# Optimization experiments

Hardware: AMD Instinct MI355X
Metric: run time of the kernel (lower is better)

Reference implementation:

```python
import jax, jax.numpy as jnp
import numpy as np
import math

# Config: 8 packed images, each a 32x32 patch grid (t=1) -> equal seglen 1024
NSEG, GH, GW = 8, 32, 32
L = GH * GW            # 1024 tokens per segment
S = NSEG * L           # 8192 packed tokens
H, NH = 1024, 16
HD = H // NH           # 64, head dim (rope dim), divisible by 4
MLP = 4096
THETA = 10000.0


def _make_rope_cos_sin():
    # Rope2DPosEmb._precompute_freqs_cis for a (GH, GW) grid, dim=HD
    flat = np.arange(L, dtype=np.float32)
    x_pos = flat % GW
    y_pos = flat // GW
    dim_range = np.arange(0, HD, 4, dtype=np.float32)[: HD // 4]
    freqs = 1.0 / THETA ** (dim_range / HD)          # [HD//4]
    x_f = np.outer(x_pos, freqs)                     # [L, HD//4]
    y_f = np.outer(y_pos, freqs)
    # interleave x/y angles per frequency -> [L, HD//2]
    ang = np.stack([x_f, y_f], axis=-1).reshape(L, HD // 2)
    ang = np.tile(ang, (NSEG, 1))                    # same grid repeated per image
    return jnp.asarray(np.cos(ang)), jnp.asarray(np.sin(ang))


def setup_inputs() -> dict:
    key = jax.random.key(0)
    ks = jax.random.split(key, 8)
    cos, sin = _make_rope_cos_sin()
    inp = {
        "x": jax.random.normal(ks[0], (S, H), jnp.float32),
        "wqkv": jax.random.normal(ks[1], (3 * H, H), jnp.float32) * math.sqrt(1.0 / H),
        "wo": jax.random.normal(ks[2], (H, H), jnp.float32) * math.sqrt(1.0 / H),
        "ln0_g": jnp.ones((H,), jnp.float32),
        "ln0_b": jnp.zeros((H,), jnp.float32),
        "ln1_g": jnp.ones((H,), jnp.float32),
        "ln1_b": jnp.zeros((H,), jnp.float32),
        "fc0_w": jax.random.normal(ks[3], (MLP, H), jnp.float32) * math.sqrt(2.0 / H),
        "fc0_b": jnp.zeros((MLP,), jnp.float32),
        "fc1_w": jax.random.normal(ks[4], (H, MLP), jnp.float32) * math.sqrt(2.0 / MLP),
        "fc1_b": jnp.zeros((H,), jnp.float32),
        "rope_cos": cos,
        "rope_sin": sin,
        "cu_seqlens": jnp.arange(NSEG + 1, dtype=jnp.int32) * L,
    }
    return inp


def _layernorm(x, g, b, eps=1e-5):
    m = x.mean(-1, keepdims=True)
    v = ((x - m) ** 2).mean(-1, keepdims=True)
    return (x - m) * jax.lax.rsqrt(v + eps) * g + b


def _apply_rope(x, cos, sin):
    # x: [S, NH, HD]; cos/sin: [S, HD//2]. Complex mult on (even, odd) pairs.
    xr = x.reshape(S, NH, HD // 2, 2)
    x0, x1 = xr[..., 0], xr[..., 1]
    c = cos[:, None, :]
    s = sin[:, None, :]
    o0 = x0 * c - x1 * s
    o1 = x0 * s + x1 * c
    return jnp.stack([o0, o1], axis=-1).reshape(S, NH, HD)


def reference(x, wqkv, wo, ln0_g, ln0_b, ln1_g, ln1_b,
              fc0_w, fc0_b, fc1_w, fc1_b, rope_cos, rope_sin, cu_seqlens):
    # --- attention branch (pre-norm) ---
    h = _layernorm(x, ln0_g, ln0_b)
    qkv = (h @ wqkv.T).reshape(S, 3, NH, HD)
    q, k, v = qkv[:, 0], qkv[:, 1], qkv[:, 2]
    q = _apply_rope(q, rope_cos, rope_sin)
    k = _apply_rope(k, rope_cos, rope_sin)
    # block-diagonal varlen attention: equal-length segments -> reshape
    qb = q.reshape(NSEG, L, NH, HD)
    kb = k.reshape(NSEG, L, NH, HD)
    vb = v.reshape(NSEG, L, NH, HD)
    scores = jnp.einsum("blhd,bmhd->bhlm", qb, kb) / math.sqrt(HD)
    p = jax.nn.softmax(scores.astype(jnp.float32), axis=-1).astype(x.dtype)
    attn = jnp.einsum("bhlm,bmhd->blhd", p, vb).reshape(S, H)
    x = x + attn @ wo.T
    # --- MLP branch (pre-norm) ---
    h2 = _layernorm(x, ln1_g, ln1_b)
    mlp = jax.nn.gelu(h2 @ fc0_w.T + fc0_b, approximate=False) @ fc1_w.T + fc1_b
    return x + mlp
```

## Files before the change

kernel.cpp:

```cpp
#include <hip/hip_runtime.h>
#include <math.h>


typedef __bf16 bf16x8 __attribute__((ext_vector_type(8)));
typedef float f32x4 __attribute__((ext_vector_type(4)));
typedef float f32x16 __attribute__((ext_vector_type(16)));
typedef unsigned int u32;

__device__ __forceinline__ unsigned short f2b(float f) {
  unsigned u = __float_as_uint(f);
  return (unsigned short)((u + 0x7FFFu + ((u >> 16) & 1u)) >> 16);
}
__device__ __forceinline__ float b2f(unsigned short h) {
  return __uint_as_float(((unsigned)h) << 16);
}
__device__ __forceinline__ void async_ld16(const void* g, void* l) {
  __builtin_amdgcn_global_load_lds((__attribute__((address_space(1))) void*)g,
                                   (__attribute__((address_space(3))) void*)l,
                                   16, 0, 0);
}
__device__ __forceinline__ float exp2fast(float x) {
#if __has_builtin(__builtin_amdgcn_exp2f)
  return __builtin_amdgcn_exp2f(x);
#else
  return exp2f(x);
#endif
}
__device__ __forceinline__ float rcpfast(float x) {
#if __has_builtin(__builtin_amdgcn_rcpf)
  return __builtin_amdgcn_rcpf(x);
#else
  return 1.0f / x;
#endif
}

__global__ __launch_bounds__(256) void castln_kernel(
    const float* __restrict__ w0, const float* __restrict__ w1,
    const float* __restrict__ w2, const float* __restrict__ w3,
    unsigned short* __restrict__ wdst,
    const float* __restrict__ x, const float* __restrict__ g,
    const float* __restrict__ bt, unsigned short* __restrict__ hout) {
  __shared__ float red[8];
  const int blk = blockIdx.x;
  if (blk < 12288) {
    const int t = blk * 256 + threadIdx.x;
    const float* src;
    int off;
    if (t < 786432) { src = w0; off = t; }
    else if (t < 1048576) { src = w1; off = t - 786432; }
    else if (t < 2097152) { src = w2; off = t - 1048576; }
    else { src = w3; off = t - 2097152; }
    const float4 v = ((const float4*)src)[off];
    ushort4 o;
    o.x = f2b(v.x); o.y = f2b(v.y); o.z = f2b(v.z); o.w = f2b(v.w);
    ((ushort4*)wdst)[t] = o;
    return;
  }
  const int row = blk - 12288, t = threadIdx.x;
  const float4 v = ((const float4*)(x + (size_t)row * 1024))[t];
  float s = v.x + v.y + v.z + v.w;
  float s2 = v.x * v.x + v.y * v.y + v.z * v.z + v.w * v.w;
#pragma unroll
  for (int m = 1; m < 64; m <<= 1) {
    s += __shfl_xor(s, m, 64);
    s2 += __shfl_xor(s2, m, 64);
  }
  if ((t & 63) == 0) { red[t >> 6] = s; red[4 + (t >> 6)] = s2; }
  __syncthreads();
  const float ts = red[0] + red[1] + red[2] + red[3];
  const float ts2 = red[4] + red[5] + red[6] + red[7];
  const float mean = ts * (1.f / 1024.f);
  const float var = ts2 * (1.f / 1024.f) - mean * mean;
  const float inv = rsqrtf(var + 1e-5f);
  const float4 gv = ((const float4*)g)[t];
  const float4 bv = ((const float4*)bt)[t];
  ushort4 o;
  o.x = f2b((v.x - mean) * inv * gv.x + bv.x);
  o.y = f2b((v.y - mean) * inv * gv.y + bv.y);
  o.z = f2b((v.z - mean) * inv * gv.z + bv.z);
  o.w = f2b((v.w - mean) * inv * gv.w + bv.w);
  ((ushort4*)hout)[(size_t)row * 256 + t] = o;
}

__global__ __launch_bounds__(256) void ln_kernel(const float* __restrict__ x,
                                                 const float* __restrict__ g,
                                                 const float* __restrict__ bt,
                                                 unsigned short* __restrict__ out) {
  __shared__ float red[8];
  const int row = blockIdx.x, t = threadIdx.x;
  const float4 v = ((const float4*)(x + (size_t)row * 1024))[t];
  float s = v.x + v.y + v.z + v.w;
  float s2 = v.x * v.x + v.y * v.y + v.z * v.z + v.w * v.w;
#pragma unroll
  for (int m = 1; m < 64; m <<= 1) {
    s += __shfl_xor(s, m, 64);
    s2 += __shfl_xor(s2, m, 64);
  }
  if ((t & 63) == 0) { red[t >> 6] = s; red[4 + (t >> 6)] = s2; }
  __syncthreads();
  const float ts = red[0] + red[1] + red[2] + red[3];
  const float ts2 = red[4] + red[5] + red[6] + red[7];
  const float mean = ts * (1.f / 1024.f);
  const float var = ts2 * (1.f / 1024.f) - mean * mean;
  const float inv = rsqrtf(var + 1e-5f);
  const float4 gv = ((const float4*)g)[t];
  const float4 bv = ((const float4*)bt)[t];
  ushort4 o;
  o.x = f2b((v.x - mean) * inv * gv.x + bv.x);
  o.y = f2b((v.y - mean) * inv * gv.y + bv.y);
  o.z = f2b((v.z - mean) * inv * gv.z + bv.z);
  o.w = f2b((v.w - mean) * inv * gv.w + bv.w);
  ((ushort4*)out)[(size_t)row * 256 + t] = o;
}

template <int MODE, int NBN, int BM>
__global__ __launch_bounds__(512, 2) void gemm_p8(
    const unsigned short* __restrict__ A, const unsigned short* __restrict__ B,
    int M, int N, int K, float* __restrict__ outf, unsigned short* __restrict__ outb,
    const float* __restrict__ res, const float* __restrict__ bias) {
  constexpr int NPH = (BM == 256) ? 4 : 2;
  constexpr int NF = (BM == 256) ? 2 : 4;
  constexpr int M_REP = BM / 32;
  constexpr int AI = BM / 128;
  constexpr int STG2 = (BM == 256) ? 2 : 1;
  __shared__ __align__(16) unsigned short As[2][2][BM * 32];
  __shared__ __align__(16) unsigned short Bs[2][2][256 * 32];
  const int bid = blockIdx.x;
  const int j8 = bid & 7, g = bid >> 3;
  const int bm = ((g / NBN) * 8 + j8) * BM;
  const int bn = (g % NBN) * 256;
  const int t = threadIdx.x, wave = t >> 6, lane = t & 63;
  const int quad = lane >> 4, l16 = lane & 15;
  const int wm = (wave >> 2) * (M_REP * 16);
  const int wn = (wave & 3) * 64;
  const int r16 = lane >> 2;
  const int cs8 = (((lane & 3) ^ ((lane >> 3) & 3)) * 8);
  const unsigned short* AgS[AI];
  unsigned short* AlS[AI];
#pragma unroll
  for (int i = 0; i < AI; i++) {
    const int r0 = wave * (AI * 16) + i * 16;
    AgS[i] = A + (size_t)(bm + r0 + r16) * K + cs8;
    AlS[i] = &As[0][0][r0 * 32];
  }
  const unsigned short* BgS[2];
  unsigned short* BlS[2];
#pragma unroll
  for (int i = 0; i < 2; i++) {
    const int r0 = wave * 32 + i * 16;
    BgS[i] = B + (size_t)(bn + r0 + r16) * K + cs8;
    BlS[i] = &Bs[0][0][r0 * 32];
  }
#define STG(bi, kt, ks)                                                      \
  do {                                                                       \
    _Pragma("unroll") for (int i_ = 0; i_ < AI; i_++)                        \
        async_ld16(AgS[i_] + (size_t)(kt) * 64 + (ks) * 32,                  \
                   AlS[i_] + ((bi) * 2 + (ks)) * (BM * 32));                 \
    _Pragma("unroll") for (int i_ = 0; i_ < 2; i_++)                         \
        async_ld16(BgS[i_] + (size_t)(kt) * 64 + (ks) * 32,                  \
                   BlS[i_] + ((bi) * 2 + (ks)) * (256 * 32));                \
  } while (0)

  f32x4 acc[M_REP][4] = {};
  const int NT = K >> 6;
  const int rq = ((quad ^ ((l16 >> 1) & 3)) * 8);
  STG(0, 0, 0);
  STG(0, 0, 1);
  STG(1, 1, 0);
  __builtin_amdgcn_sched_barrier(0);
  if (BM == 256) asm volatile("s_waitcnt vmcnt(4)" ::: "memory");
  else           asm volatile("s_waitcnt vmcnt(3)" ::: "memory");
  __builtin_amdgcn_sched_barrier(0);
  __builtin_amdgcn_s_barrier();
  __builtin_amdgcn_sched_barrier(0);

  bf16x8 af[M_REP];
  for (int u = 0; u < NT; ++u) {
    const int buf = u & 1, nbuf = buf ^ 1;
#pragma unroll
    for (int p = 0; p < NPH; ++p) {
      const int ks = (NPH == 4) ? (p >> 1) : p;
      const int j0 = (NPH == 4) ? (p & 1) * 2 : 0;
      const unsigned short* Ab = &As[buf][ks][0];
      const unsigned short* Bb = &Bs[buf][ks][0];
      if (NPH == 2 || (p & 1) == 0) {
#pragma unroll
        for (int i = 0; i < M_REP; i++)
          af[i] = *(const bf16x8*)(Ab + (wm + i * 16 + l16) * 32 + rq);
      }
      bf16x8 bfv[NF];
#pragma unroll
      for (int jj = 0; jj < NF; jj++)
        bfv[jj] = *(const bf16x8*)(Bb + (wn + (j0 + jj) * 16 + l16) * 32 + rq);
      if (p == 0 && u + 1 < NT) STG(nbuf, u + 1, 1);
      if (p == STG2 && u + 2 < NT) STG(buf, u + 2, 0);
      __builtin_amdgcn_sched_barrier(0);
      __builtin_amdgcn_s_barrier();
      asm volatile("s_waitcnt lgkmcnt(0)" ::: "memory");
      __builtin_amdgcn_sched_barrier(0);
      __builtin_amdgcn_s_setprio(1);
#pragma unroll
      for (int jj = 0; jj < NF; jj++)
#pragma unroll
        for (int i = 0; i < M_REP; i++)
          acc[i][j0 + jj] = __builtin_amdgcn_mfma_f32_16x16x32_bf16(
              af[i], bfv[jj], acc[i][j0 + jj], 0, 0, 0);
      __builtin_amdgcn_s_setprio(0);
      if (p == NPH - 1 && u + 1 < NT) {
        __builtin_amdgcn_sched_barrier(0);
        if (u + 2 < NT) {
          if (BM == 256) asm volatile("s_waitcnt vmcnt(4)" ::: "memory");
          else           asm volatile("s_waitcnt vmcnt(3)" ::: "memory");
        } else {
          asm volatile("s_waitcnt vmcnt(0)" ::: "memory");
        }
      }
      __builtin_amdgcn_sched_barrier(0);
      __builtin_amdgcn_s_barrier();
      __builtin_amdgcn_sched_barrier(0);
    }
  }
#undef STG
#pragma unroll
  for (int i = 0; i < M_REP; i++)
#pragma unroll
    for (int jj = 0; jj < 4; jj++)
#pragma unroll
      for (int r = 0; r < 4; r++) {
        const int m = bm + wm + i * 16 + quad * 4 + r;
        const int n = bn + wn + jj * 16 + l16;
        const size_t idx = (size_t)m * N + n;
        const float v = acc[i][jj][r];
        if (MODE == 1) {
          outf[idx] = v + res[idx];
        } else if (MODE == 2) {
          const float z = v + bias[n];
          const float u = z * (0.7978845608f + 0.03567740814f * z * z);
          const float e = fminf(u * 2.885390082f, 80.f);
          const float tt = exp2fast(e);
          outb[idx] = f2b(z * tt * rcpfast(tt + 1.0f));
        } else if (MODE == 3) {
          outf[idx] = v + bias[n] + res[idx];
        } else {
          outb[idx] = f2b(v);
        }
      }
}

template <int MODE, int NBN, int BN>
__global__ __launch_bounds__(512, 2) void gemm_bt8(
    const unsigned short* __restrict__ A, const unsigned short* __restrict__ B,
    int M, int N, int K, float* __restrict__ outf, unsigned short* __restrict__ outb,
    const float* __restrict__ res, const float* __restrict__ bias) {
  constexpr int NBI = BN / 64;
  constexpr int WN_WAVES = BN / 64;
  constexpr int WM_WAVES = 8 / WN_WAVES;
  constexpr int M_REP = (256 / WM_WAVES) / 16;
  constexpr int N_REP = 4;
  __shared__ __align__(16) unsigned short As[2][256 * 64];
  __shared__ __align__(16) unsigned short Bs[2][BN * 64];
  const int bid = blockIdx.x;
  const int j8 = bid & 7, g = bid >> 3;
  const int bm = ((g / NBN) * 8 + j8) * 256;
  const int bn = (g % NBN) * BN;
  const int t = threadIdx.x, wave = t >> 6, lane = t & 63;
  const int quad = lane >> 4, l16 = lane & 15;
  const int wm = (wave / WN_WAVES) * (M_REP * 16);
  const int wn = (wave % WN_WAVES) * 64;
  const int l8 = lane >> 3;
  const int cs = ((lane & 7) ^ (l8 & 7)) * 8;
  const unsigned short* Ag[4];
  unsigned short* Al[4];
#pragma unroll
  for (int i = 0; i < 4; i++) {
    const int r = wave * 32 + i * 8;
    Ag[i] = A + (size_t)(bm + r + l8) * K + cs;
    Al[i] = &As[0][r * 64];
  }
  const unsigned short* Bg[NBI];
  unsigned short* Bl[NBI];
#pragma unroll
  for (int i = 0; i < NBI; i++) {
    const int r = wave * (NBI * 8) + i * 8;
    Bg[i] = B + (size_t)(bn + r + l8) * K + cs;
    Bl[i] = &Bs[0][r * 64];
  }
#define STAGE(bi, k0)                                                        \
  do {                                                                       \
    _Pragma("unroll") for (int i_ = 0; i_ < 4; i_++)                         \
        async_ld16(Ag[i_] + (k0), Al[i_] + (bi) * (256 * 64));               \
    _Pragma("unroll") for (int i_ = 0; i_ < NBI; i_++)                       \
        async_ld16(Bg[i_] + (k0), Bl[i_] + (bi) * (BN * 64));                \
  } while (0)

  f32x4 acc[M_REP][N_REP] = {};
  const int NT = K >> 6;
  const int swk = l16 & 7;
  STAGE(0, 0);
  STAGE(1, 64);
  if (BN == 256) asm volatile("s_waitcnt vmcnt(8)" ::: "memory");
  else           asm volatile("s_waitcnt vmcnt(6)" ::: "memory");
  __builtin_amdgcn_sched_barrier(0);
  __builtin_amdgcn_s_barrier();
  __builtin_amdgcn_sched_barrier(0);
  int k0 = 128;
  for (int tI = 0; tI < NT; ++tI) {
    const int cur = tI & 1;
    const unsigned short* Ab = &As[cur][0];
    const unsigned short* Bb = &Bs[cur][0];
#pragma unroll
    for (int ks = 0; ks < 2; ks++) {
      bf16x8 af[M_REP], bfv[N_REP];
#pragma unroll
      for (int i = 0; i < M_REP; i++)
        af[i] = *(const bf16x8*)(Ab + (wm + i * 16 + l16) * 64 +
                                 (((ks * 4 + quad) ^ swk) * 8));
#pragma unroll
      for (int j = 0; j < N_REP; j++)
        bfv[j] = *(const bf16x8*)(Bb + (wn + j * 16 + l16) * 64 +
                                  (((ks * 4 + quad) ^ swk) * 8));
      __builtin_amdgcn_s_setprio(1);
#pragma unroll
      for (int j = 0; j < N_REP; j++)
#pragma unroll
        for (int i = 0; i < M_REP; i++)
          acc[i][j] = __builtin_amdgcn_mfma_f32_16x16x32_bf16(af[i], bfv[j],
                                                              acc[i][j], 0, 0, 0);
      __builtin_amdgcn_s_setprio(0);
    }
    if (tI + 1 == NT) break;
    __builtin_amdgcn_sched_barrier(0);
    __builtin_amdgcn_s_barrier();
    __builtin_amdgcn_sched_barrier(0);
    if (tI + 2 < NT) {
      STAGE(cur, k0);
      k0 += 64;
      if (BN == 256) asm volatile("s_waitcnt vmcnt(8)" ::: "memory");
      else           asm volatile("s_waitcnt vmcnt(6)" ::: "memory");
    } else {
      asm volatile("s_waitcnt vmcnt(0)" ::: "memory");
    }
    __builtin_amdgcn_sched_barrier(0);
    __builtin_amdgcn_s_barrier();
    __builtin_amdgcn_sched_barrier(0);
  }
#undef STAGE
#pragma unroll
  for (int i = 0; i < M_REP; i++)
#pragma unroll
    for (int j = 0; j < N_REP; j++)
#pragma unroll
      for (int r = 0; r < 4; r++) {
        const int m = bm + wm + i * 16 + quad * 4 + r;
        const int n = bn + wn + j * 16 + l16;
        const size_t idx = (size_t)m * N + n;
        const float v = acc[i][j][r];
        if (MODE == 1) {
          outf[idx] = v + res[idx];
        } else if (MODE == 2) {
          const float z = v + bias[n];
          const float u = z * (0.7978845608f + 0.03567740814f * z * z);
          const float e = fminf(u * 2.885390082f, 80.f);
          const float tt = exp2fast(e);
          outb[idx] = f2b(z * tt * rcpfast(tt + 1.0f));
        } else if (MODE == 3) {
          outf[idx] = v + bias[n] + res[idx];
        } else {
          outb[idx] = f2b(v);
        }
      }
}

__device__ __forceinline__ u32 rope2(u32 in, float c, float sn, float sc) {
  const float a = b2f((unsigned short)(in & 0xffff));
  const float b = b2f((unsigned short)(in >> 16));
  return (u32)f2b((a * c - b * sn) * sc) | ((u32)f2b((a * sn + b * c) * sc) << 16);
}
__global__ __launch_bounds__(256) void ropevt_kernel(const unsigned short* __restrict__ qkv,
                                                     const float* __restrict__ cb,
                                                     const float* __restrict__ sb,
                                                     unsigned short* __restrict__ qh,
                                                     unsigned short* __restrict__ kh,
                                                     unsigned short* __restrict__ vt) {
  __shared__ unsigned short tile[64][72];
  const int blk = blockIdx.x;
  if (blk < 4096) {
    const int tid = blk * 256 + threadIdx.x;
    const int ii = tid & 7, head = (tid >> 3) & 15, s = tid >> 7;
    const float4 cv = *(const float4*)(cb + s * 32 + ii * 4);
    const float4 sv = *(const float4*)(sb + s * 32 + ii * 4);
    const unsigned short* base = qkv + (size_t)s * 3072 + head * 64 + ii * 8;
    const uint4 qa = *(const uint4*)base;
    const uint4 ka = *(const uint4*)(base + 1024);
    const int seg = s >> 10, l = s & 1023;
    const size_t o = ((size_t)((seg * 16 + head) * 1024 + l)) * 64 + ii * 8;
    const float QSC = 0.125f * 1.44269504f;
    uint4 qo, ko;
    qo.x = rope2(qa.x, cv.x, sv.x, QSC); ko.x = rope2(ka.x, cv.x, sv.x, 1.f);
    qo.y = rope2(qa.y, cv.y, sv.y, QSC); ko.y = rope2(ka.y, cv.y, sv.y, 1.f);
    qo.z = rope2(qa.z, cv.z, sv.z, QSC); ko.z = rope2(ka.z, cv.z, sv.z, 1.f);
    qo.w = rope2(qa.w, cv.w, sv.w, QSC); ko.w = rope2(ka.w, cv.w, sv.w, 1.f);
    *(uint4*)(qh + o) = qo;
    *(uint4*)(kh + o) = ko;
    return;
  }
  const int b = blk - 4096;
  const int lt = b & 15, head = (b >> 4) & 15, seg = b >> 8;
  const int t = threadIdx.x;
  const int r = t >> 2, c0 = (t & 3) * 16;
  const unsigned short* src =
      qkv + ((size_t)(seg * 1024 + lt * 64 + r)) * 3072 + 2048 + head * 64 + c0;
#pragma unroll
  for (int k = 0; k < 16; k++) tile[r][c0 + k] = src[k];
  __syncthreads();
  unsigned short* dst =
      vt + ((size_t)((seg * 16 + head) * 64 + r)) * 1024 + lt * 64 + c0;
#pragma unroll
  for (int k = 0; k < 16; k++) dst[k] = tile[c0 + k][r];
}

__global__ __launch_bounds__(256) void attn_kernel(const unsigned short* __restrict__ qh,
                                                   const unsigned short* __restrict__ kh,
                                                   const unsigned short* __restrict__ vt,
                                                   unsigned short* __restrict__ out) {
  __shared__ __align__(16) unsigned short Qs[128 * 64];
  __shared__ __align__(16) unsigned short Ks[64 * 64];
  __shared__ __align__(16) unsigned short Vs[64 * 64];
  __shared__ float wl[128];
  const int b = blockIdx.x;
  const int head = b & 15, seg = (b >> 4) & 7, qt = b >> 7;
  const int t = threadIdx.x, wave = t >> 6, lane = t & 63;
  const int h = lane >> 5, q31 = lane & 31;
  const size_t sh = (size_t)(seg * 16 + head);
  const unsigned short* qbase = qh + (sh * 1024 + (size_t)qt * 128) * 64;
  const unsigned short* kbase = kh + sh * 1024 * 64;
  const unsigned short* vbase = vt + sh * 64 * 1024;
  const int r8 = lane >> 3;
  const int c8 = ((lane & 7) ^ (r8 & 7)) * 8;
#pragma unroll
  for (int cc = 0; cc < 4; cc++) {
    const int chunk = wave * 4 + cc;
    async_ld16(qbase + (size_t)(chunk * 8 + r8) * 64 + c8, Qs + chunk * 512);
  }
  const int qrow_l = wave * 32 + q31;
  const int qsw = qrow_l & 7;
  bf16x8 qf[4];
  float lsum = 0.f;
  f32x16 oacc[2] = {};

  for (int kt = 0; kt < 16; kt++) {
    const int ch0 = wave * 2;
    async_ld16(kbase + (size_t)(kt * 64 + ch0 * 8 + r8) * 64 + c8, Ks + ch0 * 512);
    async_ld16(kbase + (size_t)(kt * 64 + ch0 * 8 + 8 + r8) * 64 + c8, Ks + ch0 * 512 + 512);
    async_ld16(vbase + (size_t)(ch0 * 8 + r8) * 1024 + kt * 64 + c8, Vs + ch0 * 512);
    async_ld16(vbase + (size_t)(ch0 * 8 + 8 + r8) * 1024 + kt * 64 + c8, Vs + ch0 * 512 + 512);
    __syncthreads();
    if (kt == 0) {
#pragma unroll
      for (int ks = 0; ks < 4; ks++)
        qf[ks] = *(const bf16x8*)(Qs + qrow_l * 64 + (((2 * ks + h) ^ qsw)) * 8);
    }
    f32x16 st[2] = {{}, {}};
#pragma unroll
    for (int T = 0; T < 2; T++) {
      const int krow = 32 * T + q31;
      const int ksw = krow & 7;
#pragma unroll
      for (int ks = 0; ks < 4; ks++) {
        const bf16x8 kf = *(const bf16x8*)(Ks + krow * 64 + (((2 * ks + h) ^ ksw)) * 8);
        st[T] = __builtin_amdgcn_mfma_f32_32x32x16_bf16(kf, qf[ks], st[T], 0, 0, 0);
      }
    }
    u32 pk[2][4][2];
#pragma unroll
    for (int T = 0; T < 2; T++)
#pragma unroll
      for (int g = 0; g < 4; g++)
#pragma unroll
        for (int e = 0; e < 2; e++) {
          const float plo = exp2fast(st[T][4 * g + 2 * e]);
          const float phi = exp2fast(st[T][4 * g + 2 * e + 1]);
          lsum += plo + phi;
          pk[T][g][e] = (u32)f2b(plo) | ((u32)f2b(phi) << 16);
        }
    u32 rcv[2][4];
#pragma unroll
    for (int T = 0; T < 2; T++) {
      const u32 p0 = h ? pk[T][0][0] : pk[T][1][0];
      const u32 p1 = h ? pk[T][0][1] : pk[T][1][1];
      const u32 p2 = h ? pk[T][2][0] : pk[T][3][0];
      const u32 p3 = h ? pk[T][2][1] : pk[T][3][1];
      rcv[T][0] = (u32)__shfl_xor((int)p0, 32, 64);
      rcv[T][1] = (u32)__shfl_xor((int)p1, 32, 64);
      rcv[T][2] = (u32)__shfl_xor((int)p2, 32, 64);
      rcv[T][3] = (u32)__shfl_xor((int)p3, 32, 64);
    }
#pragma unroll
    for (int tt = 0; tt < 4; tt++) {
      const int T = tt >> 1, uu = tt & 1;
      union { u32 u[4]; bf16x8 v; } af;
      if (h == 0) {
        af.u[0] = pk[T][2 * uu][0];
        af.u[1] = pk[T][2 * uu][1];
        af.u[2] = rcv[T][2 * uu];
        af.u[3] = rcv[T][2 * uu + 1];
      } else {
        af.u[0] = rcv[T][2 * uu];
        af.u[1] = rcv[T][2 * uu + 1];
        af.u[2] = pk[T][2 * uu + 1][0];
        af.u[3] = pk[T][2 * uu + 1][1];
      }
#pragma unroll
      for (int ot = 0; ot < 2; ot++) {
        const int vrow = 32 * ot + q31;
        const int vsw = vrow & 7;
        const bf16x8 bv = *(const bf16x8*)(Vs + vrow * 64 + (((2 * tt + h) ^ vsw)) * 8);
        oacc[ot] = __builtin_amdgcn_mfma_f32_32x32x16_bf16(af.v, bv, oacc[ot], 0, 0, 0);
      }
    }
    __syncthreads();
  }
  lsum += __shfl_xor(lsum, 32, 64);
  if (h == 0) wl[wave * 32 + q31] = lsum;
  const int qglob = seg * 1024 + qt * 128 + wave * 32;
#pragma unroll
  for (int g = 0; g < 4; g++) {
    const float4 lv = *(const float4*)&wl[wave * 32 + 8 * g + 4 * h];
#pragma unroll
    for (int m = 0; m < 4; m++) {
      const int r16 = 4 * g + m;
      const int qrow = qglob + m + 8 * g + 4 * h;
      const float invl = rcpfast((&lv.x)[m]);
#pragma unroll
      for (int ot = 0; ot < 2; ot++)
        out[(size_t)qrow * 1024 + head * 64 + 32 * ot + q31] = f2b(oacc[ot][r16] * invl);
    }
  }
}

extern "C" void kernel_launch(void* const* d_in, const int* in_sizes, int n_in,
                              void* d_out, int out_size, void* d_ws, size_t ws_size,
                              hipStream_t stream) {
  (void)in_sizes; (void)n_in; (void)out_size; (void)ws_size;
  const float* x    = (const float*)d_in[0];
  const float* wqkv = (const float*)d_in[1];
  const float* wo   = (const float*)d_in[2];
  const float* ln0g = (const float*)d_in[3];
  const float* ln0b = (const float*)d_in[4];
  const float* ln1g = (const float*)d_in[5];
  const float* ln1b = (const float*)d_in[6];
  const float* fc0w = (const float*)d_in[7];
  const float* fc0b = (const float*)d_in[8];
  const float* fc1w = (const float*)d_in[9];
  const float* fc1b = (const float*)d_in[10];
  const float* rc   = (const float*)d_in[11];
  const float* rsn  = (const float*)d_in[12];
  float* out = (float*)d_out;
  char* w = (char*)d_ws;
  const size_t MB = 1u << 20;
  unsigned short* hb    = (unsigned short*)(w + 0);
  unsigned short* bqkv  = (unsigned short*)(w + 16 * MB);
  unsigned short* bwo   = (unsigned short*)(w + 22 * MB);
  unsigned short* bfc0  = (unsigned short*)(w + 24 * MB);
  unsigned short* bfc1  = (unsigned short*)(w + 32 * MB);
  unsigned short* qhb   = (unsigned short*)(w + 40 * MB);
  unsigned short* khb   = (unsigned short*)(w + 56 * MB);
  unsigned short* vtb   = (unsigned short*)(w + 72 * MB);
  unsigned short* attnb = (unsigned short*)(w + 88 * MB);
  unsigned short* qkvb  = (unsigned short*)(w + 104 * MB);
  unsigned short* midb  = (unsigned short*)(w + 104 * MB);

  castln_kernel<<<20480, 256, 0, stream>>>(wqkv, wo, fc0w, fc1w, bqkv,
                                           x, ln0g, ln0b, hb);
  gemm_p8<4, 12, 256><<<384, 512, 0, stream>>>(hb, bqkv, 8192, 3072, 1024,
                                               nullptr, qkvb, nullptr, nullptr);
  ropevt_kernel<<<6144, 256, 0, stream>>>(qkvb, rc, rsn, qhb, khb, vtb);
  attn_kernel<<<1024, 256, 0, stream>>>(qhb, khb, vtb, attnb);
  gemm_p8<1, 4, 128><<<256, 512, 0, stream>>>(attnb, bwo, 8192, 1024, 1024,
                                              out, nullptr, x, nullptr);
  ln_kernel<<<8192, 256, 0, stream>>>(out, ln1g, ln1b, hb);
  gemm_bt8<2, 16, 256><<<512, 512, 0, stream>>>(hb, bfc0, 8192, 4096, 1024,
                                                nullptr, midb, nullptr, fc0b);
  gemm_p8<3, 4, 128><<<256, 512, 0, stream>>>(midb, bfc1, 8192, 1024, 4096,
                                              out, nullptr, out, fc1b);
}
```

Before: 490.7 us.

## Double-buffer K/V tiles in attention kernel and load Q directly to registers

The attention kernel now keeps two LDS buffers for K and V and issues the asynchronous loads for the next key tile before computing on the current one. This overlaps global-to-LDS traffic with the MFMA and softmax work, and it replaces the two per-iteration __syncthreads with a single waitcnt plus barrier. Q fragments are read straight from global memory into registers, which removes the Q LDS staging buffer. LDS use stays about the same, and the raw barrier/waitcnt sequence has to be ordered correctly to avoid races.

```diff
diff --git a/kernel.cpp b/kernel.cpp
--- a/kernel.cpp
+++ b/kernel.cpp
@@ -423,9 +423,8 @@
                                                    const unsigned short* __restrict__ kh,
                                                    const unsigned short* __restrict__ vt,
                                                    unsigned short* __restrict__ out) {
-  __shared__ __align__(16) unsigned short Qs[128 * 64];
-  __shared__ __align__(16) unsigned short Ks[64 * 64];
-  __shared__ __align__(16) unsigned short Vs[64 * 64];
+  __shared__ __align__(16) unsigned short Ks[2 * 4096];
+  __shared__ __align__(16) unsigned short Vs[2 * 4096];
   __shared__ float wl[128];
   const int b = blockIdx.x;
   const int head = b & 15, seg = (b >> 4) & 7, qt = b >> 7;
@@ -437,29 +436,37 @@
   const unsigned short* vbase = vt + sh * 64 * 1024;
   const int r8 = lane >> 3;
   const int c8 = ((lane & 7) ^ (r8 & 7)) * 8;
-#pragma unroll
-  for (int cc = 0; cc < 4; cc++) {
-    const int chunk = wave * 4 + cc;
-    async_ld16(qbase + (size_t)(chunk * 8 + r8) * 64 + c8, Qs + chunk * 512);
-  }
+  const int ch0 = wave * 2;
+#define STAGEKV(kt, bi)                                                        \
+  do {                                                                         \
+    async_ld16(kbase + (size_t)((kt) * 64 + ch0 * 8 + r8) * 64 + c8,           \
+               Ks + (bi) * 4096 + ch0 * 512);                                  \
+    async_ld16(kbase + (size_t)((kt) * 64 + ch0 * 8 + 8 + r8) * 64 + c8,       \
+               Ks + (bi) * 4096 + ch0 * 512 + 512);                            \
+    async_ld16(vbase + (size_t)(ch0 * 8 + r8) * 1024 + (kt) * 64 + c8,         \
+               Vs + (bi) * 4096 + ch0 * 512);                                  \
+    async_ld16(vbase + (size_t)(ch0 * 8 + 8 + r8) * 1024 + (kt) * 64 + c8,     \
+               Vs + (bi) * 4096 + ch0 * 512 + 512);                            \
+  } while (0)
+
   const int qrow_l = wave * 32 + q31;
-  const int qsw = qrow_l & 7;
   bf16x8 qf[4];
+#pragma unroll
+  for (int ks = 0; ks < 4; ks++)
+    qf[ks] = *(const bf16x8*)(qbase + (size_t)qrow_l * 64 + ks * 16 + h * 8);
+  STAGEKV(0, 0);
+  asm volatile("s_waitcnt vmcnt(0)" ::: "memory");
+  __builtin_amdgcn_sched_barrier(0);
+  __builtin_amdgcn_s_barrier();
+  __builtin_amdgcn_sched_barrier(0);
+
   float lsum = 0.f;
   f32x16 oacc[2] = {};
-
   for (int kt = 0; kt < 16; kt++) {
-    const int ch0 = wave * 2;
-    async_ld16(kbase + (size_t)(kt * 64 + ch0 * 8 + r8) * 64 + c8, Ks + ch0 * 512);
-    async_ld16(kbase + (size_t)(kt * 64 + ch0 * 8 + 8 + r8) * 64 + c8, Ks + ch0 * 512 + 512);
-    async_ld16(vbase + (size_t)(ch0 * 8 + r8) * 1024 + kt * 64 + c8, Vs + ch0 * 512);
-    async_ld16(vbase + (size_t)(ch0 * 8 + 8 + r8) * 1024 + kt * 64 + c8, Vs + ch0 * 512 + 512);
-    __syncthreads();
-    if (kt == 0) {
-#pragma unroll
-      for (int ks = 0; ks < 4; ks++)
-        qf[ks] = *(const bf16x8*)(Qs + qrow_l * 64 + (((2 * ks + h) ^ qsw)) * 8);
-    }
+    const int cbuf = kt & 1;
+    if (kt + 1 < 16) STAGEKV(kt + 1, cbuf ^ 1);
+    const unsigned short* Kb = Ks + cbuf * 4096;
+    const unsigned short* Vb = Vs + cbuf * 4096;
     f32x16 st[2] = {{}, {}};
 #pragma unroll
     for (int T = 0; T < 2; T++) {
@@ -467,7 +474,7 @@
       const int ksw = krow & 7;
 #pragma unroll
       for (int ks = 0; ks < 4; ks++) {
-        const bf16x8 kf = *(const bf16x8*)(Ks + krow * 64 + (((2 * ks + h) ^ ksw)) * 8);
+        const bf16x8 kf = *(const bf16x8*)(Kb + krow * 64 + (((2 * ks + h) ^ ksw)) * 8);
         st[T] = __builtin_amdgcn_mfma_f32_32x32x16_bf16(kf, qf[ks], st[T], 0, 0, 0);
       }
     }
@@ -514,12 +521,19 @@
       for (int ot = 0; ot < 2; ot++) {
         const int vrow = 32 * ot + q31;
         const int vsw = vrow & 7;
-        const bf16x8 bv = *(const bf16x8*)(Vs + vrow * 64 + (((2 * tt + h) ^ vsw)) * 8);
+        const bf16x8 bv = *(const bf16x8*)(Vb + vrow * 64 + (((2 * tt + h) ^ vsw)) * 8);
         oacc[ot] = __builtin_amdgcn_mfma_f32_32x32x16_bf16(af.v, bv, oacc[ot], 0, 0, 0);
       }
     }
-    __syncthreads();
-  }
+    if (kt + 1 < 16) {
+      __builtin_amdgcn_sched_barrier(0);
+      asm volatile("s_waitcnt vmcnt(0)" ::: "memory");
+      __builtin_amdgcn_sched_barrier(0);
+      __builtin_amdgcn_s_barrier();
+      __builtin_amdgcn_sched_barrier(0);
+    }
+  }
+#undef STAGEKV
   lsum += __shfl_xor(lsum, 32, 64);
   if (h == 0) wl[wave * 32 + q31] = lsum;
   const int qglob = seg * 1024 + qt * 128 + wave * 32;
```

New measurement: 490.3 us. Within noise of the previous version (-0.1%).
